# Kernel optimization log

Measured on AMD Instinct MI355X. Metric: run time of the kernel, lower is better.

The kernel has to match this reference:

```python
import jax, jax.numpy as jnp
import numpy as np

N_HEAD = 16


def setup_inputs() -> dict:
    key = jax.random.key(0)
    ks = jax.random.split(key, 6)
    B, T, C = 2, 2048, 1024
    hs = C // N_HEAD  # 64
    block_minus_1 = 2048  # block_size - 1
    x = jax.random.normal(ks[0], (B, T, C), dtype=jnp.float32)
    W1 = jax.random.normal(ks[1], (C, C), dtype=jnp.float32) * (1.0 / np.sqrt(C))
    b1 = jnp.zeros((C,), dtype=jnp.float32)
    # original init: uniform(-1e-3, 1e-3)
    w2 = jax.random.uniform(ks[2], (hs, block_minus_1), dtype=jnp.float32, minval=-1e-3, maxval=1e-3)
    b2 = jnp.zeros((block_minus_1,), dtype=jnp.float32)
    Wv = jax.random.normal(ks[3], (C, C), dtype=jnp.float32) * (1.0 / np.sqrt(C))
    bv = jnp.zeros((C,), dtype=jnp.float32)
    Wp = jax.random.normal(ks[4], (C, C), dtype=jnp.float32) * (1.0 / np.sqrt(C))
    bp = jnp.zeros((C,), dtype=jnp.float32)
    return {"x": x, "W1": W1, "b1": b1, "w2": w2, "b2": b2,
            "Wv": Wv, "bv": bv, "Wp": Wp, "bp": bp}


def reference(x, W1, b1, w2, b2, Wv, bv, Wp, bp):
    B, T, C = x.shape
    hs = C // N_HEAD
    r = jax.nn.relu(x @ W1.T + b1).reshape(B, T, N_HEAD, hs).transpose(0, 2, 1, 3)
    # synthesizer scores: (B, nh, T, T) = relu_out @ w2[:, :T] + b2[:T]
    att = jnp.einsum('bhtd,dj->bhtj', r, w2[:, :T]) + b2[:T]
    causal = jnp.tril(jnp.ones((T, T), dtype=bool))
    att = jnp.where(causal[None, None], att, jnp.float32(-1e10))
    att = jax.nn.softmax(att, axis=-1)  # attn_drop = 0 (eval)
    v = (x @ Wv.T + bv).reshape(B, T, N_HEAD, hs).transpose(0, 2, 1, 3)
    y = jnp.einsum('bhtj,bhjd->bhtd', att, v)
    y = y.transpose(0, 2, 1, 3).reshape(B, T, C)
    return y @ Wp.T + bp  # resid_drop = 0 (eval)
```

## Files before the change

### kernel.cpp

```cpp
#include <hip/hip_runtime.h>

typedef __bf16 bf16x8 __attribute__((ext_vector_type(8)));
typedef float f32x4 __attribute__((ext_vector_type(4)));
typedef float f32x16 __attribute__((ext_vector_type(16)));

__device__ __forceinline__ unsigned short f2bf(float f) {
  union { float f; unsigned u; } v; v.f = f;
  unsigned u = v.u;
  return (unsigned short)((u + 0x7fffu + ((u >> 16) & 1u)) >> 16);
}
__device__ __forceinline__ void gload_lds16(const void* g, void* l) {
  __builtin_amdgcn_global_load_lds(
      (const __attribute__((address_space(1))) unsigned int*)g,
      (__attribute__((address_space(3))) unsigned int*)l, 16, 0, 0);
}
__device__ __forceinline__ unsigned cvtpk(float lo, float hi) {
  unsigned r;
  asm("v_cvt_pk_bf16_f32 %0, %1, %2" : "=v"(r) : "v"(lo), "v"(hi));
  return r;
}
__device__ __forceinline__ void cvt4(const float* __restrict__ s,
                                     unsigned short* __restrict__ d, int u) {
  f32x4 v = ((const f32x4*)s)[u];
  union { unsigned short s[4]; unsigned long long u; } o;
  o.s[0] = f2bf(v[0]); o.s[1] = f2bf(v[1]); o.s[2] = f2bf(v[2]); o.s[3] = f2bf(v[3]);
  ((unsigned long long*)d)[u] = o.u;
}


__global__ void prep(const float* __restrict__ x, const float* __restrict__ W1,
                     const float* __restrict__ Wv, const float* __restrict__ Wp,
                     const float* __restrict__ w2, const float* __restrict__ b2,
                     unsigned short* __restrict__ xb, unsigned short* __restrict__ W1b,
                     unsigned short* __restrict__ Wvb, unsigned short* __restrict__ Wpb,
                     unsigned short* __restrict__ w2t, unsigned short* __restrict__ ebj) {
  int u = blockIdx.x * 256 + threadIdx.x;
  if (u < 1048576) { cvt4(x, xb, u); return; }
  u -= 1048576;
  if (u < 262144) { cvt4(W1, W1b, u); return; }
  u -= 262144;
  if (u < 262144) { cvt4(Wv, Wvb, u); return; }
  u -= 262144;
  if (u < 262144) { cvt4(Wp, Wpb, u); return; }
  u -= 262144;
  if (u < 32768) {
    int j = u >> 4, d4 = (u & 15) * 4;
    union { unsigned short s[4]; unsigned long long x; } o;
#pragma unroll
    for (int i = 0; i < 4; ++i) o.s[i] = f2bf(w2[(d4 + i) * 2048 + j]);
    ((unsigned long long*)w2t)[u] = o.x;
    return;
  }
  u -= 32768;
  union { unsigned short s[4]; unsigned long long x; } o;
#pragma unroll
  for (int i = 0; i < 4; ++i) o.s[i] = f2bf(__expf(b2[u * 4 + i]));
  ((unsigned long long*)ebj)[u] = o.x;
}

__global__ __launch_bounds__(256) void gemm_rv(
    const unsigned short* __restrict__ xb, const unsigned short* __restrict__ W1b,
    const unsigned short* __restrict__ Wvb, const float* __restrict__ b1,
    const float* __restrict__ bv, const float* __restrict__ b2,
    unsigned short* __restrict__ rb, unsigned short* __restrict__ vtb) {
  __shared__ unsigned short Xs[64 * 64];
  __shared__ unsigned short W1s[64 * 64];
  __shared__ unsigned short Wvs[64 * 64];
  const int tm = blockIdx.x * 64, n0 = blockIdx.y * 64;
  const int tid = threadIdx.x;
  const int wv = tid >> 6, ln = tid & 63;
  const int l5 = ln >> 5, l31 = ln & 31;
  const int tw = (wv & 1) * 32;
  const int cw = (wv >> 1) * 32;
  const int rowL = ln >> 3;
  const int kc = (((ln & 7) ^ rowL) & 7) * 8;

  int xoff[4], woff[4];
#pragma unroll
  for (int kk = 0; kk < 4; ++kk) {
    int c = kk * 2 + l5;
    int p = (c ^ (l31 & 7)) * 8;
    xoff[kk] = (tw + l31) * 64 + p;
    woff[kk] = (cw + l31) * 64 + p;
  }

  f32x16 accR, accV;
#pragma unroll
  for (int i = 0; i < 16; ++i) { accR[i] = 0.f; accV[i] = 0.f; }

  for (int k0 = 0; k0 < 1024; k0 += 64) {
    __syncthreads();
#pragma unroll
    for (int l = 0; l < 2; ++l) {
      int row = l * 32 + wv * 8 + rowL;
      gload_lds16(xb + (tm + row) * 1024 + k0 + kc, &Xs[l * 2048 + wv * 512]);
      gload_lds16(W1b + (n0 + row) * 1024 + k0 + kc, &W1s[l * 2048 + wv * 512]);
      gload_lds16(Wvb + (n0 + row) * 1024 + k0 + kc, &Wvs[l * 2048 + wv * 512]);
    }
    __syncthreads();
#pragma unroll
    for (int kk = 0; kk < 4; ++kk) {
      bf16x8 xa  = *(const bf16x8*)&Xs[xoff[kk]];
      bf16x8 w1f = *(const bf16x8*)&W1s[woff[kk]];
      bf16x8 wvf = *(const bf16x8*)&Wvs[woff[kk]];
      accR = __builtin_amdgcn_mfma_f32_32x32x16_bf16(xa, w1f, accR, 0, 0, 0);
      accV = __builtin_amdgcn_mfma_f32_32x32x16_bf16(wvf, xa, accV, 0, 0, 0);
    }
  }
  {
    int col = n0 + cw + l31;
    float bc = b1[col];
#pragma unroll
    for (int r = 0; r < 16; ++r) {
      int rr = (r & 3) + 8 * (r >> 2) + 4 * l5;
      float v = accR[r] + bc;
      rb[(tm + tw + rr) * 1024 + col] = f2bf(v > 0.f ? v : 0.f);
    }
  }
  {
    int tok = tm + tw + l31;
    float eb = __expf(b2[tok & 2047]);
#pragma unroll
    for (int r = 0; r < 16; ++r) {
      int rr = (r & 3) + 8 * (r >> 2) + 4 * l5;
      int ch = n0 + cw + rr;
      vtb[ch * 4096 + tok] = f2bf((accV[r] + bv[ch]) * eb);
    }
  }
}

__global__ __launch_bounds__(256) void gemm_p(
    const unsigned short* __restrict__ A, const unsigned short* __restrict__ Bt,
    const float* __restrict__ bias, float* __restrict__ C) {
  __shared__ unsigned short As[64 * 128];
  __shared__ unsigned short Bs[64 * 128];
  const int tid = threadIdx.x;
  const int wv = tid >> 6, ln = tid & 63;
  const int l5 = ln >> 5, l31 = ln & 31;
  const int wm = (wv & 1) * 32, wn = (wv >> 1) * 32;
  const int tileM = blockIdx.y * 64, tileN = blockIdx.x * 64;
  const int srow = ln >> 4, pos = ln & 15;

  int aoff[8], boff[8];
#pragma unroll
  for (int kk = 0; kk < 8; ++kk) {
    int c = kk * 2 + l5;
    int p = ((c & 8) | ((c & 7) ^ (l31 & 7))) * 8;
    aoff[kk] = (wm + l31) * 128 + p;
    boff[kk] = (wn + l31) * 128 + p;
  }

  f32x16 acc;
#pragma unroll
  for (int i = 0; i < 16; ++i) acc[i] = 0.f;

  for (int k0 = 0; k0 < 1024; k0 += 128) {
    __syncthreads();
#pragma unroll
    for (int l = 0; l < 4; ++l) {
      int row = l * 16 + wv * 4 + srow;
      int cs = (pos & 8) | ((pos & 7) ^ (row & 7));
      gload_lds16(A + (tileM + row) * 1024 + k0 + cs * 8, &As[(l * 16 + wv * 4) * 128]);
      gload_lds16(Bt + (tileN + row) * 1024 + k0 + cs * 8, &Bs[(l * 16 + wv * 4) * 128]);
    }
    __syncthreads();
#pragma unroll
    for (int kk = 0; kk < 8; ++kk) {
      bf16x8 af  = *(const bf16x8*)&As[aoff[kk]];
      bf16x8 bfr = *(const bf16x8*)&Bs[boff[kk]];
      acc = __builtin_amdgcn_mfma_f32_32x32x16_bf16(af, bfr, acc, 0, 0, 0);
    }
  }
#pragma unroll
  for (int r = 0; r < 16; ++r) {
    int rr = (r & 3) + 8 * (r >> 2) + 4 * l5;
    int row = tileM + wm + rr;
    int col = tileN + wn + l31;
    C[row * 1024 + col] = acc[r] + bias[col];
  }
}

__global__ __launch_bounds__(256, 2) void attn(
    const unsigned short* __restrict__ r, const unsigned short* __restrict__ w2t,
    const unsigned short* __restrict__ vt, const unsigned short* __restrict__ ebj,
    unsigned short* __restrict__ y) {
  __shared__ unsigned short W2s[2][64 * 64];
  __shared__ unsigned short Vs[2][64 * 64];

  const int tid = threadIdx.x;
  const int wv = tid >> 6, ln = tid & 63;
  const int quad = ln >> 4, lq = ln & 15;
  const int bh = blockIdx.x, b = bh >> 4, h = bh & 15;
  const int q = blockIdx.y;
  const int p = (q < 8) ? q : 23 - q;
  const int ta = p, tb = 31 - p;
  const int t0a = ta * 64, t0b = tb * 64;
  const int rowL = ln >> 3;
  const int kc = (((ln & 7) ^ rowL) & 7) * 8;
  const int sx = lq & 7;
  const int ko0 = (quad ^ sx) * 8, ko1 = ((4 + quad) ^ sx) * 8;

  bf16x8 ra[2][2];
  {
    const unsigned short* base = r + (b * 2048 + wv * 16 + lq) * 1024 + h * 64 + quad * 8;
    ra[0][0] = *(const bf16x8*)(base + t0a * 1024);
    ra[0][1] = *(const bf16x8*)(base + t0a * 1024 + 32);
    ra[1][0] = *(const bf16x8*)(base + t0b * 1024);
    ra[1][1] = *(const bf16x8*)(base + t0b * 1024 + 32);
  }

  f32x4 accY[2][4];
  f32x4 accL[2];
  const f32x4 zf = {0.f, 0.f, 0.f, 0.f};
#pragma unroll
  for (int s = 0; s < 2; ++s) {
    accL[s] = zf;
#pragma unroll
    for (int nd = 0; nd < 4; ++nd) accY[s][nd] = zf;
  }

  auto stage = [&](int jt, int bi) {
    int j0 = jt * 64;
#pragma unroll
    for (int l = 0; l < 2; ++l) {
      int row = l * 32 + wv * 8 + rowL;
      gload_lds16(w2t + (j0 + row) * 64 + kc, &W2s[bi][l * 2048 + wv * 512]);
      gload_lds16(vt + (h * 64 + row) * 4096 + b * 2048 + j0 + kc,
                  &Vs[bi][l * 2048 + wv * 512]);
    }
  };

#define TILE(S, T0, TT)                                                         \
    {                                                                           \
      f32x4 sv[4];                                                              \
      _Pragma("unroll") for (int ni = 0; ni < 4; ++ni) {                        \
        sv[ni] = __builtin_amdgcn_mfma_f32_16x16x32_bf16(w2f0[ni], ra[S][0], zf, 0, 0, 0); \
        sv[ni] = __builtin_amdgcn_mfma_f32_16x16x32_bf16(w2f1[ni], ra[S][1], sv[ni], 0, 0, 0); \
      }                                                                         \
      const bool diag = (jt == (TT));                                           \
      const int tl = (T0) + wv * 16 + lq;                                       \
      _Pragma("unroll") for (int ni = 0; ni < 4; ++ni)                          \
        _Pragma("unroll") for (int rg = 0; rg < 4; ++rg) {                      \
          float pe = __expf(sv[ni][rg]);                                        \
          if (diag) {                                                           \
            int j = j0 + ni * 16 + quad * 4 + rg;                               \
            pe = (j <= tl) ? pe : 0.f;                                          \
          }                                                                     \
          sv[ni][rg] = pe;                                                      \
        }                                                                       \
      bf16x8 pa0, pa1;                                                          \
      {                                                                         \
        union { unsigned u[4]; bf16x8 v; } k0u, k1u;                            \
        _Pragma("unroll") for (int pr = 0; pr < 2; ++pr) {                      \
          unsigned a0 = cvtpk(sv[0][2 * pr], sv[0][2 * pr + 1]);                \
          unsigned b0 = cvtpk(sv[1][2 * pr], sv[1][2 * pr + 1]);                \
          asm("v_permlane32_swap_b32 %0, %1" : "+v"(a0), "+v"(b0));             \
          asm("v_permlane16_swap_b32 %0, %1" : "+v"(a0), "+v"(b0));             \
          k0u.u[pr] = a0; k0u.u[2 + pr] = b0;                                   \
          unsigned a1 = cvtpk(sv[2][2 * pr], sv[2][2 * pr + 1]);                \
          unsigned b1 = cvtpk(sv[3][2 * pr], sv[3][2 * pr + 1]);                \
          asm("v_permlane32_swap_b32 %0, %1" : "+v"(a1), "+v"(b1));             \
          asm("v_permlane16_swap_b32 %0, %1" : "+v"(a1), "+v"(b1));             \
          k1u.u[pr] = a1; k1u.u[2 + pr] = b1;                                   \
        }                                                                       \
        pa0 = k0u.v; pa1 = k1u.v;                                               \
      }                                                                         \
      _Pragma("unroll") for (int nd = 0; nd < 4; ++nd) {                        \
        bf16x8 bb0 = *(const bf16x8*)&Vs[cb][(nd * 16 + lq) * 64 + ko0];        \
        accY[S][nd] = __builtin_amdgcn_mfma_f32_16x16x32_bf16(pa0, bb0, accY[S][nd], 0, 0, 0); \
        bf16x8 bb1 = *(const bf16x8*)&Vs[cb][(nd * 16 + lq) * 64 + ko1];        \
        accY[S][nd] = __builtin_amdgcn_mfma_f32_16x16x32_bf16(pa1, bb1, accY[S][nd], 0, 0, 0); \
      }                                                                         \
      accL[S] = __builtin_amdgcn_mfma_f32_16x16x32_bf16(pa0, eb0, accL[S], 0, 0, 0); \
      accL[S] = __builtin_amdgcn_mfma_f32_16x16x32_bf16(pa1, eb1, accL[S], 0, 0, 0); \
    }

#define WRITEOUT(S, T0)                                                         \
    {                                                                           \
      float inv[4];                                                             \
      _Pragma("unroll") for (int rg = 0; rg < 4; ++rg)                          \
        inv[rg] = __builtin_amdgcn_rcpf(accL[S][rg]);                           \
      _Pragma("unroll") for (int nd = 0; nd < 4; ++nd)                          \
        _Pragma("unroll") for (int rg = 0; rg < 4; ++rg) {                      \
          int t = (T0) + wv * 16 + quad * 4 + rg;                               \
          y[(b * 2048 + t) * 1024 + h * 64 + nd * 16 + lq] =                    \
              f2bf(accY[S][nd][rg] * inv[rg]);                                  \
        }                                                                       \
    }

  stage(0, 0);
  for (int jt = 0; jt <= tb; ++jt) {
    const int cb = jt & 1;
    __syncthreads();
    if (jt < tb) stage(jt + 1, cb ^ 1);
    const int j0 = jt * 64;

    bf16x8 eb0 = *(const bf16x8*)&ebj[j0 + quad * 8];
    bf16x8 eb1 = *(const bf16x8*)&ebj[j0 + 32 + quad * 8];
    bf16x8 w2f0[4], w2f1[4];
#pragma unroll
    for (int ni = 0; ni < 4; ++ni) {
      w2f0[ni] = *(const bf16x8*)&W2s[cb][(ni * 16 + lq) * 64 + ko0];
      w2f1[ni] = *(const bf16x8*)&W2s[cb][(ni * 16 + lq) * 64 + ko1];
    }

    if (jt <= ta) TILE(0, t0a, ta);
    TILE(1, t0b, tb);
    if (jt == ta) WRITEOUT(0, t0a);
  }
  WRITEOUT(1, t0b);
#undef TILE
#undef WRITEOUT
}

extern "C" void kernel_launch(void* const* d_in, const int* in_sizes, int n_in,
                              void* d_out, int out_size, void* d_ws, size_t ws_size,
                              hipStream_t stream) {
  const float* x  = (const float*)d_in[0];
  const float* W1 = (const float*)d_in[1];
  const float* b1 = (const float*)d_in[2];
  const float* w2 = (const float*)d_in[3];
  const float* b2 = (const float*)d_in[4];
  const float* Wv = (const float*)d_in[5];
  const float* bv = (const float*)d_in[6];
  const float* Wp = (const float*)d_in[7];
  const float* bp = (const float*)d_in[8];

  unsigned short* ws  = (unsigned short*)d_ws;
  unsigned short* xb   = ws;
  unsigned short* W1b  = ws + 4194304;
  unsigned short* Wvb  = ws + 5242880;
  unsigned short* Wpb  = ws + 6291456;
  unsigned short* w2t  = ws + 7340032;
  unsigned short* rb   = ws + 7471104;
  unsigned short* vt   = ws + 11665408;
  unsigned short* yb   = ws + 15859712;
  unsigned short* ebjb = ws + 20054016;

  prep<<<7298, 256, 0, stream>>>(x, W1, Wv, Wp, w2, b2, xb, W1b, Wvb, Wpb, w2t, ebjb);
  gemm_rv<<<dim3(64, 16), 256, 0, stream>>>(xb, W1b, Wvb, b1, bv, b2, rb, vt);
  attn<<<dim3(32, 16), 256, 0, stream>>>(rb, w2t, vt, ebjb, yb);
  gemm_p<<<dim3(16, 64), 256, 0, stream>>>(yb, Wpb, bp, (float*)d_out);
}
```

Before: 166.3 us.

## Double-buffer LDS staging in projection GEMMs with one barrier per k-step

Both the fused r/v projection GEMM and the output projection GEMM now use two LDS buffers. The global-to-LDS load for the next k-tile is issued before the MFMAs on the current tile, so the loads overlap with the math, and each k-step needs one barrier instead of two. The output GEMM also drops its k-tile from 128 to 64 to match the doubled buffers and keep LDS use the same. Occupancy hints are added to the launch bounds (3 and 4 blocks per CU). The cost is more LDS per block in gemm_rv and a possible rise in register pressure under the occupancy hints.

```diff
diff --git a/kernel.cpp b/kernel.cpp
--- a/kernel.cpp
+++ b/kernel.cpp
@@ -58,14 +58,14 @@
   ((unsigned long long*)ebj)[u] = o.x;
 }
 
-__global__ __launch_bounds__(256) void gemm_rv(
+__global__ __launch_bounds__(256, 3) void gemm_rv(
     const unsigned short* __restrict__ xb, const unsigned short* __restrict__ W1b,
     const unsigned short* __restrict__ Wvb, const float* __restrict__ b1,
     const float* __restrict__ bv, const float* __restrict__ b2,
     unsigned short* __restrict__ rb, unsigned short* __restrict__ vtb) {
-  __shared__ unsigned short Xs[64 * 64];
-  __shared__ unsigned short W1s[64 * 64];
-  __shared__ unsigned short Wvs[64 * 64];
+  __shared__ unsigned short Xs[2][64 * 64];
+  __shared__ unsigned short W1s[2][64 * 64];
+  __shared__ unsigned short Wvs[2][64 * 64];
   const int tm = blockIdx.x * 64, n0 = blockIdx.y * 64;
   const int tid = threadIdx.x;
   const int wv = tid >> 6, ln = tid & 63;
@@ -84,25 +84,30 @@
     woff[kk] = (cw + l31) * 64 + p;
   }
 
-  f32x16 accR, accV;
-#pragma unroll
-  for (int i = 0; i < 16; ++i) { accR[i] = 0.f; accV[i] = 0.f; }
-
-  for (int k0 = 0; k0 < 1024; k0 += 64) {
-    __syncthreads();
+  auto stage = [&](int k0, int bi) {
 #pragma unroll
     for (int l = 0; l < 2; ++l) {
       int row = l * 32 + wv * 8 + rowL;
-      gload_lds16(xb + (tm + row) * 1024 + k0 + kc, &Xs[l * 2048 + wv * 512]);
-      gload_lds16(W1b + (n0 + row) * 1024 + k0 + kc, &W1s[l * 2048 + wv * 512]);
-      gload_lds16(Wvb + (n0 + row) * 1024 + k0 + kc, &Wvs[l * 2048 + wv * 512]);
-    }
+      gload_lds16(xb + (tm + row) * 1024 + k0 + kc, &Xs[bi][l * 2048 + wv * 512]);
+      gload_lds16(W1b + (n0 + row) * 1024 + k0 + kc, &W1s[bi][l * 2048 + wv * 512]);
+      gload_lds16(Wvb + (n0 + row) * 1024 + k0 + kc, &Wvs[bi][l * 2048 + wv * 512]);
+    }
+  };
+
+  f32x16 accR, accV;
+#pragma unroll
+  for (int i = 0; i < 16; ++i) { accR[i] = 0.f; accV[i] = 0.f; }
+
+  stage(0, 0);
+  for (int it = 0; it < 16; ++it) {
+    const int cb = it & 1;
     __syncthreads();
+    if (it < 15) stage((it + 1) * 64, cb ^ 1);
 #pragma unroll
     for (int kk = 0; kk < 4; ++kk) {
-      bf16x8 xa  = *(const bf16x8*)&Xs[xoff[kk]];
-      bf16x8 w1f = *(const bf16x8*)&W1s[woff[kk]];
-      bf16x8 wvf = *(const bf16x8*)&Wvs[woff[kk]];
+      bf16x8 xa  = *(const bf16x8*)&Xs[cb][xoff[kk]];
+      bf16x8 w1f = *(const bf16x8*)&W1s[cb][woff[kk]];
+      bf16x8 wvf = *(const bf16x8*)&Wvs[cb][woff[kk]];
       accR = __builtin_amdgcn_mfma_f32_32x32x16_bf16(xa, w1f, accR, 0, 0, 0);
       accV = __builtin_amdgcn_mfma_f32_32x32x16_bf16(wvf, xa, accV, 0, 0, 0);
     }
@@ -129,45 +134,50 @@
   }
 }
 
-__global__ __launch_bounds__(256) void gemm_p(
+__global__ __launch_bounds__(256, 4) void gemm_p(
     const unsigned short* __restrict__ A, const unsigned short* __restrict__ Bt,
     const float* __restrict__ bias, float* __restrict__ C) {
-  __shared__ unsigned short As[64 * 128];
-  __shared__ unsigned short Bs[64 * 128];
+  __shared__ unsigned short As[2][64 * 64];
+  __shared__ unsigned short Bs[2][64 * 64];
   const int tid = threadIdx.x;
   const int wv = tid >> 6, ln = tid & 63;
   const int l5 = ln >> 5, l31 = ln & 31;
   const int wm = (wv & 1) * 32, wn = (wv >> 1) * 32;
   const int tileM = blockIdx.y * 64, tileN = blockIdx.x * 64;
-  const int srow = ln >> 4, pos = ln & 15;
-
-  int aoff[8], boff[8];
-#pragma unroll
-  for (int kk = 0; kk < 8; ++kk) {
+  const int rowL = ln >> 3;
+  const int kc = (((ln & 7) ^ rowL) & 7) * 8;
+
+  int aoff[4], boff[4];
+#pragma unroll
+  for (int kk = 0; kk < 4; ++kk) {
     int c = kk * 2 + l5;
-    int p = ((c & 8) | ((c & 7) ^ (l31 & 7))) * 8;
-    aoff[kk] = (wm + l31) * 128 + p;
-    boff[kk] = (wn + l31) * 128 + p;
-  }
+    int p = (c ^ (l31 & 7)) * 8;
+    aoff[kk] = (wm + l31) * 64 + p;
+    boff[kk] = (wn + l31) * 64 + p;
+  }
+
+  auto stage = [&](int k0, int bi) {
+#pragma unroll
+    for (int l = 0; l < 2; ++l) {
+      int row = l * 32 + wv * 8 + rowL;
+      gload_lds16(A + (tileM + row) * 1024 + k0 + kc, &As[bi][l * 2048 + wv * 512]);
+      gload_lds16(Bt + (tileN + row) * 1024 + k0 + kc, &Bs[bi][l * 2048 + wv * 512]);
+    }
+  };
 
   f32x16 acc;
 #pragma unroll
   for (int i = 0; i < 16; ++i) acc[i] = 0.f;
 
-  for (int k0 = 0; k0 < 1024; k0 += 128) {
+  stage(0, 0);
+  for (int it = 0; it < 16; ++it) {
+    const int cb = it & 1;
     __syncthreads();
-#pragma unroll
-    for (int l = 0; l < 4; ++l) {
-      int row = l * 16 + wv * 4 + srow;
-      int cs = (pos & 8) | ((pos & 7) ^ (row & 7));
-      gload_lds16(A + (tileM + row) * 1024 + k0 + cs * 8, &As[(l * 16 + wv * 4) * 128]);
-      gload_lds16(Bt + (tileN + row) * 1024 + k0 + cs * 8, &Bs[(l * 16 + wv * 4) * 128]);
-    }
-    __syncthreads();
-#pragma unroll
-    for (int kk = 0; kk < 8; ++kk) {
-      bf16x8 af  = *(const bf16x8*)&As[aoff[kk]];
-      bf16x8 bfr = *(const bf16x8*)&Bs[boff[kk]];
+    if (it < 15) stage((it + 1) * 64, cb ^ 1);
+#pragma unroll
+    for (int kk = 0; kk < 4; ++kk) {
+      bf16x8 af  = *(const bf16x8*)&As[cb][aoff[kk]];
+      bf16x8 bfr = *(const bf16x8*)&Bs[cb][boff[kk]];
       acc = __builtin_amdgcn_mfma_f32_32x32x16_bf16(af, bfr, acc, 0, 0, 0);
     }
   }
```

Result: slower. 185.3 us (+11.5%).

## Split paired causal query tiles into one tile per block, heaviest first

Applied to the files above, without the earlier changes.

The attention kernel previously had each block process two query tiles (p and 31-p) so that every block did balanced work. Each block now handles a single 64-row query tile. The grid doubles to 32x32 and blockIdx.y is reversed so the longest tiles launch first. Launch bounds rise to 4 blocks per CU, which cuts per-thread register state and is meant to raise occupancy and latency hiding. In exchange, W2/V tiles are loaded once per query tile instead of being shared across the pair, so LDS staging traffic roughly doubles, and load balance now depends on the hardware scheduler.

```diff
diff --git a/kernel.cpp b/kernel.cpp
--- a/kernel.cpp
+++ b/kernel.cpp
@@ -180,7 +180,7 @@
   }
 }
 
-__global__ __launch_bounds__(256, 2) void attn(
+__global__ __launch_bounds__(256, 4) void attn(
     const unsigned short* __restrict__ r, const unsigned short* __restrict__ w2t,
     const unsigned short* __restrict__ vt, const unsigned short* __restrict__ ebj,
     unsigned short* __restrict__ y) {
@@ -191,33 +191,28 @@
   const int wv = tid >> 6, ln = tid & 63;
   const int quad = ln >> 4, lq = ln & 15;
   const int bh = blockIdx.x, b = bh >> 4, h = bh & 15;
-  const int q = blockIdx.y;
-  const int p = (q < 8) ? q : 23 - q;
-  const int ta = p, tb = 31 - p;
-  const int t0a = ta * 64, t0b = tb * 64;
+  const int q = 31 - blockIdx.y;
+  const int t0 = q * 64;
+  const int NB = q + 1;
   const int rowL = ln >> 3;
   const int kc = (((ln & 7) ^ rowL) & 7) * 8;
   const int sx = lq & 7;
   const int ko0 = (quad ^ sx) * 8, ko1 = ((4 + quad) ^ sx) * 8;
 
-  bf16x8 ra[2][2];
+  bf16x8 ra0, ra1;
   {
-    const unsigned short* base = r + (b * 2048 + wv * 16 + lq) * 1024 + h * 64 + quad * 8;
-    ra[0][0] = *(const bf16x8*)(base + t0a * 1024);
-    ra[0][1] = *(const bf16x8*)(base + t0a * 1024 + 32);
-    ra[1][0] = *(const bf16x8*)(base + t0b * 1024);
-    ra[1][1] = *(const bf16x8*)(base + t0b * 1024 + 32);
-  }
-
-  f32x4 accY[2][4];
-  f32x4 accL[2];
+    const unsigned short* base =
+        r + (b * 2048 + t0 + wv * 16 + lq) * 1024 + h * 64 + quad * 8;
+    ra0 = *(const bf16x8*)(base);
+    ra1 = *(const bf16x8*)(base + 32);
+  }
+
+  f32x4 accY[4];
+  f32x4 accL;
   const f32x4 zf = {0.f, 0.f, 0.f, 0.f};
-#pragma unroll
-  for (int s = 0; s < 2; ++s) {
-    accL[s] = zf;
-#pragma unroll
-    for (int nd = 0; nd < 4; ++nd) accY[s][nd] = zf;
-  }
+  accL = zf;
+#pragma unroll
+  for (int nd = 0; nd < 4; ++nd) accY[nd] = zf;
 
   auto stage = [&](int jt, int bi) {
     int j0 = jt * 64;
@@ -230,69 +225,11 @@
     }
   };
 
-#define TILE(S, T0, TT)                                                         \
-    {                                                                           \
-      f32x4 sv[4];                                                              \
-      _Pragma("unroll") for (int ni = 0; ni < 4; ++ni) {                        \
-        sv[ni] = __builtin_amdgcn_mfma_f32_16x16x32_bf16(w2f0[ni], ra[S][0], zf, 0, 0, 0); \
-        sv[ni] = __builtin_amdgcn_mfma_f32_16x16x32_bf16(w2f1[ni], ra[S][1], sv[ni], 0, 0, 0); \
-      }                                                                         \
-      const bool diag = (jt == (TT));                                           \
-      const int tl = (T0) + wv * 16 + lq;                                       \
-      _Pragma("unroll") for (int ni = 0; ni < 4; ++ni)                          \
-        _Pragma("unroll") for (int rg = 0; rg < 4; ++rg) {                      \
-          float pe = __expf(sv[ni][rg]);                                        \
-          if (diag) {                                                           \
-            int j = j0 + ni * 16 + quad * 4 + rg;                               \
-            pe = (j <= tl) ? pe : 0.f;                                          \
-          }                                                                     \
-          sv[ni][rg] = pe;                                                      \
-        }                                                                       \
-      bf16x8 pa0, pa1;                                                          \
-      {                                                                         \
-        union { unsigned u[4]; bf16x8 v; } k0u, k1u;                            \
-        _Pragma("unroll") for (int pr = 0; pr < 2; ++pr) {                      \
-          unsigned a0 = cvtpk(sv[0][2 * pr], sv[0][2 * pr + 1]);                \
-          unsigned b0 = cvtpk(sv[1][2 * pr], sv[1][2 * pr + 1]);                \
-          asm("v_permlane32_swap_b32 %0, %1" : "+v"(a0), "+v"(b0));             \
-          asm("v_permlane16_swap_b32 %0, %1" : "+v"(a0), "+v"(b0));             \
-          k0u.u[pr] = a0; k0u.u[2 + pr] = b0;                                   \
-          unsigned a1 = cvtpk(sv[2][2 * pr], sv[2][2 * pr + 1]);                \
-          unsigned b1 = cvtpk(sv[3][2 * pr], sv[3][2 * pr + 1]);                \
-          asm("v_permlane32_swap_b32 %0, %1" : "+v"(a1), "+v"(b1));             \
-          asm("v_permlane16_swap_b32 %0, %1" : "+v"(a1), "+v"(b1));             \
-          k1u.u[pr] = a1; k1u.u[2 + pr] = b1;                                   \
-        }                                                                       \
-        pa0 = k0u.v; pa1 = k1u.v;                                               \
-      }                                                                         \
-      _Pragma("unroll") for (int nd = 0; nd < 4; ++nd) {                        \
-        bf16x8 bb0 = *(const bf16x8*)&Vs[cb][(nd * 16 + lq) * 64 + ko0];        \
-        accY[S][nd] = __builtin_amdgcn_mfma_f32_16x16x32_bf16(pa0, bb0, accY[S][nd], 0, 0, 0); \
-        bf16x8 bb1 = *(const bf16x8*)&Vs[cb][(nd * 16 + lq) * 64 + ko1];        \
-        accY[S][nd] = __builtin_amdgcn_mfma_f32_16x16x32_bf16(pa1, bb1, accY[S][nd], 0, 0, 0); \
-      }                                                                         \
-      accL[S] = __builtin_amdgcn_mfma_f32_16x16x32_bf16(pa0, eb0, accL[S], 0, 0, 0); \
-      accL[S] = __builtin_amdgcn_mfma_f32_16x16x32_bf16(pa1, eb1, accL[S], 0, 0, 0); \
-    }
-
-#define WRITEOUT(S, T0)                                                         \
-    {                                                                           \
-      float inv[4];                                                             \
-      _Pragma("unroll") for (int rg = 0; rg < 4; ++rg)                          \
-        inv[rg] = __builtin_amdgcn_rcpf(accL[S][rg]);                           \
-      _Pragma("unroll") for (int nd = 0; nd < 4; ++nd)                          \
-        _Pragma("unroll") for (int rg = 0; rg < 4; ++rg) {                      \
-          int t = (T0) + wv * 16 + quad * 4 + rg;                               \
-          y[(b * 2048 + t) * 1024 + h * 64 + nd * 16 + lq] =                    \
-              f2bf(accY[S][nd][rg] * inv[rg]);                                  \
-        }                                                                       \
-    }
-
   stage(0, 0);
-  for (int jt = 0; jt <= tb; ++jt) {
+  for (int jt = 0; jt < NB; ++jt) {
     const int cb = jt & 1;
     __syncthreads();
-    if (jt < tb) stage(jt + 1, cb ^ 1);
+    if (jt + 1 < NB) stage(jt + 1, cb ^ 1);
     const int j0 = jt * 64;
 
     bf16x8 eb0 = *(const bf16x8*)&ebj[j0 + quad * 8];
@@ -304,13 +241,69 @@
       w2f1[ni] = *(const bf16x8*)&W2s[cb][(ni * 16 + lq) * 64 + ko1];
     }
 
-    if (jt <= ta) TILE(0, t0a, ta);
-    TILE(1, t0b, tb);
-    if (jt == ta) WRITEOUT(0, t0a);
-  }
-  WRITEOUT(1, t0b);
-#undef TILE
-#undef WRITEOUT
+    f32x4 sv[4];
+#pragma unroll
+    for (int ni = 0; ni < 4; ++ni) {
+      sv[ni] = __builtin_amdgcn_mfma_f32_16x16x32_bf16(w2f0[ni], ra0, zf, 0, 0, 0);
+      sv[ni] = __builtin_amdgcn_mfma_f32_16x16x32_bf16(w2f1[ni], ra1, sv[ni], 0, 0, 0);
+    }
+    const bool diag = (jt == NB - 1);
+    const int tl = t0 + wv * 16 + lq;
+#pragma unroll
+    for (int ni = 0; ni < 4; ++ni)
+#pragma unroll
+      for (int rg = 0; rg < 4; ++rg) {
+        float pe = __expf(sv[ni][rg]);
+        if (diag) {
+          int j = j0 + ni * 16 + quad * 4 + rg;
+          pe = (j <= tl) ? pe : 0.f;
+        }
+        sv[ni][rg] = pe;
+      }
+
+    bf16x8 pa0, pa1;
+    {
+      union { unsigned u[4]; bf16x8 v; } k0u, k1u;
+#pragma unroll
+      for (int pr = 0; pr < 2; ++pr) {
+        unsigned a0 = cvtpk(sv[0][2 * pr], sv[0][2 * pr + 1]);
+        unsigned b0 = cvtpk(sv[1][2 * pr], sv[1][2 * pr + 1]);
+        asm("v_permlane32_swap_b32 %0, %1" : "+v"(a0), "+v"(b0));
+        asm("v_permlane16_swap_b32 %0, %1" : "+v"(a0), "+v"(b0));
+        k0u.u[pr] = a0; k0u.u[2 + pr] = b0;
+        unsigned a1 = cvtpk(sv[2][2 * pr], sv[2][2 * pr + 1]);
+        unsigned b1 = cvtpk(sv[3][2 * pr], sv[3][2 * pr + 1]);
+        asm("v_permlane32_swap_b32 %0, %1" : "+v"(a1), "+v"(b1));
+        asm("v_permlane16_swap_b32 %0, %1" : "+v"(a1), "+v"(b1));
+        k1u.u[pr] = a1; k1u.u[2 + pr] = b1;
+      }
+      pa0 = k0u.v; pa1 = k1u.v;
+    }
+
+#pragma unroll
+    for (int nd = 0; nd < 4; ++nd) {
+      bf16x8 bb0 = *(const bf16x8*)&Vs[cb][(nd * 16 + lq) * 64 + ko0];
+      accY[nd] = __builtin_amdgcn_mfma_f32_16x16x32_bf16(pa0, bb0, accY[nd], 0, 0, 0);
+      bf16x8 bb1 = *(const bf16x8*)&Vs[cb][(nd * 16 + lq) * 64 + ko1];
+      accY[nd] = __builtin_amdgcn_mfma_f32_16x16x32_bf16(pa1, bb1, accY[nd], 0, 0, 0);
+    }
+    accL = __builtin_amdgcn_mfma_f32_16x16x32_bf16(pa0, eb0, accL, 0, 0, 0);
+    accL = __builtin_amdgcn_mfma_f32_16x16x32_bf16(pa1, eb1, accL, 0, 0, 0);
+  }
+
+  {
+    float inv[4];
+#pragma unroll
+    for (int rg = 0; rg < 4; ++rg) inv[rg] = __builtin_amdgcn_rcpf(accL[rg]);
+#pragma unroll
+    for (int nd = 0; nd < 4; ++nd)
+#pragma unroll
+      for (int rg = 0; rg < 4; ++rg) {
+        int t = t0 + wv * 16 + quad * 4 + rg;
+        y[(b * 2048 + t) * 1024 + h * 64 + nd * 16 + lq] =
+            f2bf(accY[nd][rg] * inv[rg]);
+      }
+  }
 }
 
 extern "C" void kernel_launch(void* const* d_in, const int* in_sizes, int n_in,
@@ -339,6 +332,6 @@
 
   prep<<<7298, 256, 0, stream>>>(x, W1, Wv, Wp, w2, b2, xb, W1b, Wvb, Wpb, w2t, ebjb);
   gemm_rv<<<dim3(64, 16), 256, 0, stream>>>(xb, W1b, Wvb, b1, bv, b2, rb, vt);
-  attn<<<dim3(32, 16), 256, 0, stream>>>(rb, w2t, vt, ebjb, yb);
+  attn<<<dim3(32, 32), 256, 0, stream>>>(rb, w2t, vt, ebjb, yb);
   gemm_p<<<dim3(16, 64), 256, 0, stream>>>(yb, Wpb, bp, (float*)d_out);
 }
```

After: 171.2 us. 2.9% more time.
